# Kernel optimization log

Hardware: AMD Instinct MI355X
Metric: run time of the kernel (lower is better)

Reference implementation:

```python
import jax, jax.numpy as jnp
import numpy as np

N_NODES = 100000
N_EDGES = 1600000
N_GRAPHS = 256
HIDDEN = 128
IN_FEAT = 5


def setup_inputs() -> dict:
    key = jax.random.key(0)
    ks = jax.random.split(key, 12)
    x = jax.random.normal(ks[0], (N_NODES, IN_FEAT), dtype=jnp.float32)
    edge_index = jax.random.randint(ks[1], (2, N_EDGES), 0, N_NODES, dtype=jnp.int64)
    batch = jnp.sort(jax.random.randint(ks[2], (N_NODES,), 0, N_GRAPHS, dtype=jnp.int64))
    s = 0.05
    W0 = jax.random.normal(ks[3], (IN_FEAT, HIDDEN), dtype=jnp.float32) * s
    b0 = jnp.zeros((HIDDEN,), dtype=jnp.float32)
    W1 = jax.random.normal(ks[4], (HIDDEN, HIDDEN), dtype=jnp.float32) * s
    b1 = jnp.zeros((HIDDEN,), dtype=jnp.float32)
    W2 = jax.random.normal(ks[5], (HIDDEN, HIDDEN), dtype=jnp.float32) * s
    b2 = jnp.zeros((HIDDEN,), dtype=jnp.float32)
    lin_w = jax.random.normal(ks[6], (HIDDEN, 1), dtype=jnp.float32) * s
    lin_b = jnp.zeros((1,), dtype=jnp.float32)
    return {"x": x, "edge_index": edge_index, "batch": batch,
            "W0": W0, "b0": b0, "W1": W1, "b1": b1, "W2": W2, "b2": b2,
            "lin_w": lin_w, "lin_b": lin_b}


def reference(x, edge_index, batch, W0, b0, W1, b1, W2, b2, lin_w, lin_b):
    n = x.shape[0]
    # PyG GCNConv: add self-loops, symmetric normalization D^-1/2 (A+I) D^-1/2
    loop = jnp.arange(n, dtype=edge_index.dtype)
    src = jnp.concatenate([edge_index[0], loop])  # [E+N]
    dst = jnp.concatenate([edge_index[1], loop])
    deg = jax.ops.segment_sum(jnp.ones_like(dst, dtype=x.dtype), dst, num_segments=n)
    dis = jnp.where(deg > 0, jax.lax.rsqrt(jnp.maximum(deg, 1.0)), 0.0)
    norm = (dis[src] * dis[dst])[:, None]  # [E+N, 1]

    def gcn_conv(h, W, b):
        h = h @ W                      # [N, H]
        msg = h[src] * norm            # gather + scale, [E+N, H]
        return jax.ops.segment_sum(msg, dst, num_segments=n) + b

    h = jax.nn.relu(gcn_conv(x, W0, b0))
    h = jax.nn.relu(gcn_conv(h, W1, b1))
    h = gcn_conv(h, W2, b2)

    # global_mean_pool over batch ids
    sums = jax.ops.segment_sum(h, batch, num_segments=N_GRAPHS)
    cnt = jax.ops.segment_sum(jnp.ones((n,), x.dtype), batch, num_segments=N_GRAPHS)
    g = sums / jnp.maximum(cnt, 1.0)[:, None]
    # dropout p=0.01 is identity in eval mode
    return jax.nn.sigmoid(g @ lin_w + lin_b)  # [N_GRAPHS, 1]
```

## Files before the change

kernel.cpp:

```cpp
#include <hip/hip_runtime.h>
#include <hip/hip_fp8.h>

#define GCN_N 100000
#define GCN_H 128
#define GCN_G 256
#define NPB_SHIFT 9
#define NPB 512
#define NBKT 196
#define CHUNK 2048
#define SRC_BITS 17
#define SRC_MASK ((1 << SRC_BITS) - 1)
#define T1_SCALE 256.0f
#define T1_INV_SCALE (1.0f / 256.0f)

static_assert(GCN_N < (1 << SRC_BITS), "src id must fit 17 bits");

using short8 = __attribute__((ext_vector_type(8))) short;
using f32x4  = __attribute__((ext_vector_type(4))) float;
using f32x2  = __attribute__((ext_vector_type(2))) float;

#if defined(__has_builtin)
#if __has_builtin(__builtin_amdgcn_cvt_pk_f32_fp8) && __has_builtin(__builtin_amdgcn_cvt_pk_fp8_f32)
#define HW_FP8 1
#endif
#endif


__device__ __forceinline__ unsigned short f2bf(float f) {
    unsigned u = __float_as_uint(f);
    unsigned r = u + 0x7FFFu + ((u >> 16) & 1u);
    return (unsigned short)(r >> 16);
}
__device__ __forceinline__ float bf2f(unsigned short h) {
    return __uint_as_float(((unsigned)h) << 16);
}

__device__ __forceinline__ void fp8x4_to_f32(unsigned v, float* f) {
#ifdef HW_FP8
    f32x2 lo = __builtin_amdgcn_cvt_pk_f32_fp8((int)v, false);
    f32x2 hi = __builtin_amdgcn_cvt_pk_f32_fp8((int)v, true);
    f[0] = lo[0]; f[1] = lo[1]; f[2] = hi[0]; f[3] = hi[1];
#else
    #pragma unroll
    for (int j = 0; j < 4; j++) {
        __hip_fp8_e4m3 h;
        h.__x = (unsigned char)((v >> (8 * j)) & 0xFF);
        f[j] = (float)h;
    }
#endif
}

__device__ __forceinline__ unsigned f32x4_to_fp8(float f0, float f1, float f2, float f3) {
#ifdef HW_FP8
    int r = __builtin_amdgcn_cvt_pk_fp8_f32(f0, f1, 0, false);
    r = __builtin_amdgcn_cvt_pk_fp8_f32(f2, f3, r, true);
    return (unsigned)r;
#else
    unsigned r = 0;
    float ff[4] = {f0, f1, f2, f3};
    #pragma unroll
    for (int j = 0; j < 4; j++) {
        __hip_fp8_e4m3 h(ff[j]);
        r |= ((unsigned)h.__x) << (8 * j);
    }
    return r;
#endif
}


__global__ __launch_bounds__(256) void hist_kernel(const int* __restrict__ dst,
                                                   int* __restrict__ hist, int E) {
    __shared__ int lh[NBKT];
    int tid = threadIdx.x;
    if (tid < NBKT) lh[tid] = 0;
    __syncthreads();
    int e0 = blockIdx.x * CHUNK;
    #pragma unroll
    for (int i = 0; i < CHUNK / 256; i++) {
        int e = e0 + tid + i * 256;
        if (e < E) atomicAdd(&lh[dst[e] >> NPB_SHIFT], 1);
    }
    __syncthreads();
    if (tid < NBKT) hist[(size_t)blockIdx.x * NBKT + tid] = lh[tid];
}

__global__ __launch_bounds__(64) void scan_cols_kernel(const int* __restrict__ hist,
                                                       int* __restrict__ offsT,
                                                       int* __restrict__ btot, int B) {
    int k = blockIdx.x;
    int lane = threadIdx.x;
    int running = 0;
    for (int b0 = 0; b0 < B; b0 += 64) {
        int b = b0 + lane;
        int v = (b < B) ? hist[(size_t)b * NBKT + k] : 0;
        int iv = v;
        #pragma unroll
        for (int d = 1; d < 64; d <<= 1) {
            int x = __shfl_up(iv, d, 64);
            if (lane >= d) iv += x;
        }
        if (b < B) offsT[(size_t)k * B + b] = running + iv - v;
        running += __shfl(iv, 63, 64);
    }
    if (lane == 0) btot[k] = running;
}

__global__ void bucket_base_kernel(const int* __restrict__ btot,
                                   int* __restrict__ bbase,
                                   int* __restrict__ rowptr, int n) {
    if (threadIdx.x == 0 && blockIdx.x == 0) {
        int run = 0;
        for (int i = 0; i < NBKT; i++) { bbase[i] = run; run += btot[i]; }
        bbase[NBKT] = run;
        rowptr[n] = run;
    }
}

__global__ __launch_bounds__(256) void partition_kernel(const int* __restrict__ src,
                                                        const int* __restrict__ dst,
                                                        const int* __restrict__ bbase,
                                                        const int* __restrict__ offsT,
                                                        int* __restrict__ epack,
                                                        int E, int B) {
    __shared__ int cur[NBKT];
    int blk = blockIdx.x, tid = threadIdx.x;
    if (tid < NBKT) cur[tid] = bbase[tid] + offsT[(size_t)tid * B + blk];
    __syncthreads();
    int e0 = blk * CHUNK;
    #pragma unroll
    for (int i = 0; i < CHUNK / 256; i++) {
        int e = e0 + tid + i * 256;
        if (e < E) {
            int d = dst[e];
            int s = src[e];
            int pos = atomicAdd(&cur[d >> NPB_SHIFT], 1);
            epack[pos] = ((d & (NPB - 1)) << SRC_BITS) | s;
        }
    }
}

__global__ __launch_bounds__(512) void csr_build_kernel(const int* __restrict__ epack,
                                                        const int* __restrict__ bbase,
                                                        const float* __restrict__ x,
                                                        int* __restrict__ rowptr,
                                                        float* __restrict__ dis,
                                                        float* __restrict__ xsp,
                                                        int* __restrict__ csrc, int n) {
    __shared__ int lcount[NPB];
    __shared__ int lcur[NPB];
    __shared__ int wsums[8];
    int k = blockIdx.x, tid = threadIdx.x;
    int lane = tid & 63, wid = tid >> 6;
    int nodebase = k << NPB_SHIFT;
    int ebeg = bbase[k], eend = bbase[k + 1];

    lcount[tid] = 0;
    __syncthreads();
    for (int e = ebeg + tid; e < eend; e += 512)
        atomicAdd(&lcount[epack[e] >> SRC_BITS], 1);
    __syncthreads();

    int v = lcount[tid];
    int iv = v;
    #pragma unroll
    for (int d = 1; d < 64; d <<= 1) {
        int x2 = __shfl_up(iv, d, 64);
        if (lane >= d) iv += x2;
    }
    if (lane == 63) wsums[wid] = iv;
    __syncthreads();
    if (tid == 0) {
        int r = 0;
        #pragma unroll
        for (int w = 0; w < 8; w++) { int t = wsums[w]; wsums[w] = r; r += t; }
    }
    __syncthreads();
    int ex = wsums[wid] + iv - v;
    lcur[tid] = ex;
    int node = nodebase + tid;
    if (node < n) {
        rowptr[node] = ebeg + ex;
        float dd = rsqrtf((float)(v + 1));
        dis[node] = dd;
        const float* xr = x + (size_t)node * 5;
        float4 a;
        a.x = xr[0] * dd; a.y = xr[1] * dd; a.z = xr[2] * dd; a.w = xr[3] * dd;
        float a4 = xr[4] * dd;
        ((float4*)(xsp + (size_t)node * 8))[0] = a;
        xsp[(size_t)node * 8 + 4] = a4;
        xsp[(size_t)node * 8 + 5] = 0.f;
        xsp[(size_t)node * 8 + 6] = 0.f;
        xsp[(size_t)node * 8 + 7] = 0.f;
    }
    __syncthreads();
    for (int e = ebeg + tid; e < eend; e += 512) {
        int p = epack[e];
        int pos = atomicAdd(&lcur[p >> SRC_BITS], 1);
        csrc[ebeg + pos] = p & SRC_MASK;
    }
}


__global__ __launch_bounds__(256) void aggx_kernel(const float* __restrict__ xsp,
                                                   const float* __restrict__ dis,
                                                   const int* __restrict__ rowptr,
                                                   const int* __restrict__ csrc,
                                                   float* __restrict__ a0p, int n) {
    int i = blockIdx.x * 256 + threadIdx.x;
    if (i >= n) return;
    float4 acc = ((const float4*)(xsp + (size_t)i * 8))[0];
    float acc4 = xsp[(size_t)i * 8 + 4];
    int r0 = rowptr[i], r1 = rowptr[i + 1];
    int e = r0;
    for (; e + 3 < r1; e += 4) {
        int s0 = csrc[e], s1 = csrc[e + 1], s2 = csrc[e + 2], s3 = csrc[e + 3];
        float4 v0 = ((const float4*)(xsp + (size_t)s0 * 8))[0];
        float a40 = xsp[(size_t)s0 * 8 + 4];
        float4 v1 = ((const float4*)(xsp + (size_t)s1 * 8))[0];
        float a41 = xsp[(size_t)s1 * 8 + 4];
        float4 v2 = ((const float4*)(xsp + (size_t)s2 * 8))[0];
        float a42 = xsp[(size_t)s2 * 8 + 4];
        float4 v3 = ((const float4*)(xsp + (size_t)s3 * 8))[0];
        float a43 = xsp[(size_t)s3 * 8 + 4];
        acc.x += (v0.x + v1.x) + (v2.x + v3.x);
        acc.y += (v0.y + v1.y) + (v2.y + v3.y);
        acc.z += (v0.z + v1.z) + (v2.z + v3.z);
        acc.w += (v0.w + v1.w) + (v2.w + v3.w);
        acc4  += (a40 + a41) + (a42 + a43);
    }
    for (; e < r1; e++) {
        int s = csrc[e];
        float4 v = ((const float4*)(xsp + (size_t)s * 8))[0];
        acc.x += v.x; acc.y += v.y; acc.z += v.z; acc.w += v.w;
        acc4 += xsp[(size_t)s * 8 + 4];
    }
    float di = dis[i];
    acc.x *= di; acc.y *= di; acc.z *= di; acc.w *= di; acc4 *= di;
    ((float4*)(a0p + (size_t)i * 8))[0] = acc;
    a0p[(size_t)i * 8 + 4] = acc4;
}


__global__ __launch_bounds__(256) void w2l_kernel(const float* __restrict__ W2,
                                                  const float* __restrict__ b2,
                                                  const float* __restrict__ lw,
                                                  float* __restrict__ w2l,
                                                  float* __restrict__ c2) {
    __shared__ float slw[128];
    int tid = threadIdx.x;
    if (tid < 128) slw[tid] = lw[tid];
    __syncthreads();
    if (tid < 128) {
        float s = 0.f;
        #pragma unroll 8
        for (int j = 0; j < 128; j++) s = fmaf(W2[tid * 128 + j], slw[j], s);
        w2l[tid] = s;
    } else if (tid == 128) {
        float s = 0.f;
        for (int j = 0; j < 128; j++) s = fmaf(b2[j], slw[j], s);
        c2[0] = s;
    }
}

__global__ __launch_bounds__(256) void w1cvt_kernel(const float* __restrict__ W1,
                                                    unsigned short* __restrict__ w1t) {
    int idx = blockIdx.x * 256 + threadIdx.x;
    int col = idx >> 7, k = idx & 127;
    w1t[idx] = f2bf(W1[k * 128 + col]);
}


__global__ __launch_bounds__(256) void mmfused_kernel(const float* __restrict__ a0p,
                                                      const float* __restrict__ W0,
                                                      const float* __restrict__ b0,
                                                      const unsigned short* __restrict__ w1t,
                                                      const float* __restrict__ dis,
                                                      unsigned* __restrict__ t1f8, int n) {
    __shared__ __align__(16) unsigned short sA[128 * 128];
    __shared__ __align__(16) unsigned short sBT[128 * 128];
    __shared__ __align__(16) float4 sA0[256];
    __shared__ float sDis[128];
    char* sAb = (char*)sA;
    char* sBb = (char*)sBT;
    int tid = threadIdx.x;
    int rowBase = blockIdx.x * 128;

    {
        int rowL = tid >> 1, q = tid & 1;
        int gr = rowBase + rowL;
        float4 v = make_float4(0.f, 0.f, 0.f, 0.f);
        if (gr < n) v = ((const float4*)a0p)[(size_t)gr * 2 + q];
        sA0[tid] = v;
        if (tid < 128) {
            int g2 = rowBase + tid;
            sDis[tid] = (g2 < n) ? dis[g2] : 0.f;
        }
    }
    #pragma unroll
    for (int it = 0; it < 8; it++) {
        int idx = tid + it * 256;
        int col = idx >> 4, c = idx & 15;
        uint4 v = ((const uint4*)w1t)[idx];
        int byteoff = (col * 256 + c * 16) ^ ((col & 7) << 4);
        *(uint4*)(sBb + byteoff) = v;
    }
    __syncthreads();

    {
        int cq = tid & 31;
        int rg = tid >> 5;
        float4 w0q[5];
        #pragma unroll
        for (int j = 0; j < 5; j++) w0q[j] = *((const float4*)(W0 + j * 128 + cq * 4));
        float4 b0q = *((const float4*)(b0 + cq * 4));
        const float* sA0f = (const float*)sA0;
        #pragma unroll
        for (int ri = 0; ri < 16; ri++) {
            int row = rg + ri * 8;
            const float* ar = sA0f + row * 8;
            float4 h = b0q;
            #pragma unroll
            for (int j = 0; j < 5; j++) {
                float aj = ar[j];
                h.x = fmaf(aj, w0q[j].x, h.x);
                h.y = fmaf(aj, w0q[j].y, h.y);
                h.z = fmaf(aj, w0q[j].z, h.z);
                h.w = fmaf(aj, w0q[j].w, h.w);
            }
            h.x = fmaxf(h.x, 0.f); h.y = fmaxf(h.y, 0.f);
            h.z = fmaxf(h.z, 0.f); h.w = fmaxf(h.w, 0.f);
            uint2 p;
            p.x = (unsigned)f2bf(h.x) | ((unsigned)f2bf(h.y) << 16);
            p.y = (unsigned)f2bf(h.z) | ((unsigned)f2bf(h.w) << 16);
            int byteoff = (row * 256 + cq * 8) ^ ((row & 7) << 4);
            *(uint2*)(sAb + byteoff) = p;
        }
    }
    __syncthreads();

    int wave = tid >> 6, l = tid & 63;
    int lr = l & 15, lg = l >> 4;
    int rb = wave * 32;

    short8 afr[2][4];
    #pragma unroll
    for (int rt = 0; rt < 2; rt++) {
        int row = rb + rt * 16 + lr;
        #pragma unroll
        for (int ks = 0; ks < 4; ks++) {
            int byteoff = (row * 256 + ks * 64 + lg * 16) ^ ((row & 7) << 4);
            afr[rt][ks] = *(const short8*)(sAb + byteoff);
        }
    }
    f32x4 acc[2][8];
    #pragma unroll
    for (int rt = 0; rt < 2; rt++)
        #pragma unroll
        for (int ct = 0; ct < 8; ct++)
            acc[rt][ct] = (f32x4){0.f, 0.f, 0.f, 0.f};

    #pragma unroll
    for (int ct = 0; ct < 8; ct++) {
        int col = ct * 16 + lr;
        short8 bfr[4];
        #pragma unroll
        for (int ks = 0; ks < 4; ks++) {
            int byteoff = (col * 256 + ks * 64 + lg * 16) ^ ((col & 7) << 4);
            bfr[ks] = *(const short8*)(sBb + byteoff);
        }
        #pragma unroll
        for (int rt = 0; rt < 2; rt++) {
            #pragma unroll
            for (int ks = 0; ks < 4; ks++) {
                acc[rt][ct] = __builtin_amdgcn_mfma_f32_16x16x32_bf16(
                    afr[rt][ks], bfr[ks], acc[rt][ct], 0, 0, 0);
            }
        }
    }

    #pragma unroll
    for (int rt = 0; rt < 2; rt++) {
        #pragma unroll
        for (int i = 0; i < 4; i++) {
            int rowL = rb + rt * 16 + lg * 4 + i;
            float dsc = sDis[rowL] * T1_SCALE;
            #pragma unroll
            for (int ct = 0; ct < 8; ct++) {
                int col = ct * 16 + lr;
                int byteoff = (rowL * 256 + col * 2) ^ ((rowL & 7) << 4);
                *(unsigned short*)(sAb + byteoff) = f2bf(acc[rt][ct][i] * dsc);
            }
        }
    }
    __syncthreads();

    #pragma unroll
    for (int it = 0; it < 8; it++) {
        int flat = tid + it * 256;
        int rowL = flat >> 4, c16 = flat & 15;
        int gr = rowBase + rowL;
        if (gr < n) {
            int byteoff = (rowL * 256 + c16 * 16) ^ ((rowL & 7) << 4);
            uint4 v = *(const uint4*)(sAb + byteoff);
            float f0 = __uint_as_float(v.x << 16), f1 = __uint_as_float(v.x & 0xFFFF0000u);
            float f2 = __uint_as_float(v.y << 16), f3 = __uint_as_float(v.y & 0xFFFF0000u);
            float f4 = __uint_as_float(v.z << 16), f5 = __uint_as_float(v.z & 0xFFFF0000u);
            float f6 = __uint_as_float(v.w << 16), f7 = __uint_as_float(v.w & 0xFFFF0000u);
            uint2 p;
            p.x = f32x4_to_fp8(f0, f1, f2, f3);
            p.y = f32x4_to_fp8(f4, f5, f6, f7);
            ((uint2*)t1f8)[(size_t)gr * 16 + c16] = p;
        }
    }
}


__global__ __launch_bounds__(256) void agg1_kernel(const unsigned* __restrict__ t1f8,
                                                   const float* __restrict__ dis,
                                                   const int* __restrict__ rowptr,
                                                   const int* __restrict__ csrc,
                                                   const float* __restrict__ b1,
                                                   const float* __restrict__ w2l,
                                                   float* __restrict__ z, int n) {
    int group = threadIdx.x >> 4, lane = threadIdx.x & 15;
    int i = blockIdx.x * 16 + group;
    if (i >= n) return;
    const uint2* t2 = (const uint2*)t1f8;
    float f[8];
    uint2 sv = t2[(size_t)i * 16 + lane];
    fp8x4_to_f32(sv.x, f);
    fp8x4_to_f32(sv.y, f + 4);
    float acc[8];
    #pragma unroll
    for (int j = 0; j < 8; j++) acc[j] = f[j];
    int r0 = rowptr[i], r1 = rowptr[i + 1];
    int e = r0;
    for (; e + 7 < r1; e += 8) {
        uint2 vv[8];
        #pragma unroll
        for (int u = 0; u < 8; u++) vv[u] = t2[(size_t)csrc[e + u] * 16 + lane];
        #pragma unroll
        for (int u = 0; u < 8; u++) {
            fp8x4_to_f32(vv[u].x, f);
            fp8x4_to_f32(vv[u].y, f + 4);
            #pragma unroll
            for (int j = 0; j < 8; j++) acc[j] += f[j];
        }
    }
    for (; e < r1; e++) {
        uint2 v = t2[(size_t)csrc[e] * 16 + lane];
        fp8x4_to_f32(v.x, f);
        fp8x4_to_f32(v.y, f + 4);
        #pragma unroll
        for (int j = 0; j < 8; j++) acc[j] += f[j];
    }
    float di = dis[i];
    float dis_s = di * T1_INV_SCALE;
    float4 b4a = ((const float4*)b1)[lane * 2];
    float4 b4b = ((const float4*)b1)[lane * 2 + 1];
    float4 w4a = ((const float4*)w2l)[lane * 2];
    float4 w4b = ((const float4*)w2l)[lane * 2 + 1];
    float bb[8] = {b4a.x, b4a.y, b4a.z, b4a.w, b4b.x, b4b.y, b4b.z, b4b.w};
    float ww[8] = {w4a.x, w4a.y, w4a.z, w4a.w, w4b.x, w4b.y, w4b.z, w4b.w};
    float d = 0.f;
    #pragma unroll
    for (int j = 0; j < 8; j++) {
        float c = fmaxf(fmaf(dis_s, acc[j], bb[j]), 0.f);
        d = fmaf(c, ww[j], d);
    }
    #pragma unroll
    for (int o = 8; o > 0; o >>= 1) d += __shfl_down(d, o, 16);
    if (lane == 0) z[i] = di * d;
}


__global__ __launch_bounds__(256) void aggz_pool_kernel(const float* __restrict__ z,
                                                        const float* __restrict__ dis,
                                                        const int* __restrict__ rowptr,
                                                        const int* __restrict__ csrc,
                                                        const int* __restrict__ batch,
                                                        float* __restrict__ gsum, int n) {
    __shared__ float lg[GCN_G];
    int tid = threadIdx.x;
    lg[tid] = 0.f;
    __syncthreads();
    int i = blockIdx.x * 256 + tid;
    float ndv = 0.f;
    int g = 0;
    if (i < n) {
        float acc = z[i];
        int r0 = rowptr[i], r1 = rowptr[i + 1];
        int e = r0;
        for (; e + 3 < r1; e += 4) {
            acc += (z[csrc[e]] + z[csrc[e + 1]]) + (z[csrc[e + 2]] + z[csrc[e + 3]]);
        }
        for (; e < r1; e++) acc += z[csrc[e]];
        ndv = dis[i] * acc;
        g = batch[i];
    }
    int lane = tid & 63;
    int g0 = __shfl(g, 0, 64);
    bool uni = __all(g == g0);
    if (uni) {
        float s = ndv;
        #pragma unroll
        for (int o = 32; o > 0; o >>= 1) s += __shfl_down(s, o, 64);
        if (lane == 0 && s != 0.f) atomicAdd(&lg[g0], s);
    } else {
        if (ndv != 0.f) atomicAdd(&lg[g], ndv);
    }
    __syncthreads();
    float v = lg[tid];
    if (v != 0.f) atomicAdd(&gsum[tid], v);
}


__global__ __launch_bounds__(256) void boundary_kernel(const int* __restrict__ batch,
                                                       int* __restrict__ gstart, int n) {
    int i = blockIdx.x * 256 + threadIdx.x;
    if (i >= n) return;
    int b = batch[i];
    int pb = (i == 0) ? -1 : batch[i - 1];
    for (int g = pb + 1; g <= b; g++) gstart[g] = i;
    if (i == n - 1) {
        for (int g = b + 1; g <= GCN_G; g++) gstart[g] = n;
    }
}

__global__ __launch_bounds__(256) void final_kernel(const float* __restrict__ gsum,
                                                    const int* __restrict__ gstart,
                                                    const float* __restrict__ c2,
                                                    const float* __restrict__ lb,
                                                    float* __restrict__ out) {
    int g = threadIdx.x;
    float cnt = (float)max(gstart[g + 1] - gstart[g], 1);
    float v = gsum[g] / cnt + c2[0] + lb[0];
    out[g] = 1.f / (1.f + expf(-v));
}


extern "C" void kernel_launch(void* const* d_in, const int* in_sizes, int n_in,
                              void* d_out, int out_size, void* d_ws, size_t ws_size,
                              hipStream_t stream) {
    const float* x   = (const float*)d_in[0];
    const int*   ei  = (const int*)d_in[1];
    const int*   bat = (const int*)d_in[2];
    const float* W0  = (const float*)d_in[3];
    const float* b0  = (const float*)d_in[4];
    const float* W1  = (const float*)d_in[5];
    const float* b1  = (const float*)d_in[6];
    const float* W2  = (const float*)d_in[7];
    const float* b2  = (const float*)d_in[8];
    const float* lw  = (const float*)d_in[9];
    const float* lb  = (const float*)d_in[10];
    float* out = (float*)d_out;

    const int N = GCN_N;
    const int E = in_sizes[1] / 2;
    const int B = (E + CHUNK - 1) / CHUNK;

    char* ws = (char*)d_ws;
    size_t off = 0;
    auto alloc = [&](size_t bytes) {
        size_t o = off;
        off += (bytes + 255) & ~(size_t)255;
        return o;
    };
    int*   hist    = (int*)(ws + alloc((size_t)B * NBKT * 4));
    int*   offsT   = (int*)(ws + alloc((size_t)NBKT * B * 4));
    int*   btot    = (int*)(ws + alloc((size_t)NBKT * 4));
    int*   bbase   = (int*)(ws + alloc((size_t)(NBKT + 1) * 4));
    int*   epack   = (int*)(ws + alloc((size_t)E * 4));
    int*   rowptr  = (int*)(ws + alloc((size_t)(N + 1) * 4));
    float* dis     = (float*)(ws + alloc((size_t)N * 4));
    int*   csrc    = (int*)(ws + alloc((size_t)E * 4));
    float* xsp     = (float*)(ws + alloc((size_t)N * 8 * 4));
    float* a0p     = (float*)(ws + alloc((size_t)N * 8 * 4));
    unsigned* t1f8 = (unsigned*)(ws + alloc((size_t)N * GCN_H));
    float* z       = (float*)(ws + alloc((size_t)N * 4));
    int*   gstart  = (int*)(ws + alloc((size_t)(GCN_G + 1) * 4));
    float* w2l     = (float*)(ws + alloc(128 * 4));
    float* c2      = (float*)(ws + alloc(4));
    unsigned short* w1t = (unsigned short*)(ws + alloc(128 * 128 * 2));
    float* gsum    = (float*)(ws + alloc(GCN_G * 4));

    const int* src = ei;
    const int* dst = ei + E;

    hipMemsetAsync(gsum, 0, GCN_G * 4, stream);

    hist_kernel<<<B, 256, 0, stream>>>(dst, hist, E);
    scan_cols_kernel<<<NBKT, 64, 0, stream>>>(hist, offsT, btot, B);
    bucket_base_kernel<<<1, 64, 0, stream>>>(btot, bbase, rowptr, N);
    partition_kernel<<<B, 256, 0, stream>>>(src, dst, bbase, offsT, epack, E, B);
    csr_build_kernel<<<NBKT, 512, 0, stream>>>(epack, bbase, x, rowptr, dis, xsp, csrc, N);
    boundary_kernel<<<(N + 255) / 256, 256, 0, stream>>>(bat, gstart, N);
    w2l_kernel<<<1, 256, 0, stream>>>(W2, b2, lw, w2l, c2);
    w1cvt_kernel<<<64, 256, 0, stream>>>(W1, w1t);

    aggx_kernel<<<(N + 255) / 256, 256, 0, stream>>>(xsp, dis, rowptr, csrc, a0p, N);
    mmfused_kernel<<<(N + 127) / 128, 256, 0, stream>>>(a0p, W0, b0, w1t, dis, t1f8, N);
    agg1_kernel<<<(N + 15) / 16, 256, 0, stream>>>(t1f8, dis, rowptr, csrc, b1, w2l, z, N);
    aggz_pool_kernel<<<(N + 255) / 256, 256, 0, stream>>>(z, dis, rowptr, csrc, bat, gsum, N);

    final_kernel<<<1, 256, 0, stream>>>(gsum, gstart, c2, lb, out);
}
```

Measured before the change: 152.0 us.

## Merge prep kernels, cache edges in LDS, widen gather unrolls, count graphs in pool

Merges the W1 conversion, W2·lin_w reduction and bucket-base scan into one prep kernel, and drops boundary_kernel by counting nodes per graph inside the pooling kernel, so fewer kernels are launched. csr_build now caches its bucket's packed edges in LDS to avoid a second global read, at the cost of 40KB of shared memory per block, which may lower occupancy. The aggregation loops gather 8 or 16 neighbours per step, and agg1 loads indices cooperatively and broadcasts them with shuffles, to raise memory-level parallelism. The extra gcnt buffer relies on being allocated right after gsum so that the widened memset clears both.

```diff
diff --git a/kernel.cpp b/kernel.cpp
--- a/kernel.cpp
+++ b/kernel.cpp
@@ -12,6 +12,7 @@
 #define SRC_MASK ((1 << SRC_BITS) - 1)
 #define T1_SCALE 256.0f
 #define T1_INV_SCALE (1.0f / 256.0f)
+#define EBUF_CAP 10240
 
 static_assert(GCN_N < (1 << SRC_BITS), "src id must fit 17 bits");
 
@@ -105,14 +106,42 @@
     if (lane == 0) btot[k] = running;
 }
 
-__global__ void bucket_base_kernel(const int* __restrict__ btot,
-                                   int* __restrict__ bbase,
-                                   int* __restrict__ rowptr, int n) {
-    if (threadIdx.x == 0 && blockIdx.x == 0) {
-        int run = 0;
-        for (int i = 0; i < NBKT; i++) { bbase[i] = run; run += btot[i]; }
-        bbase[NBKT] = run;
-        rowptr[n] = run;
+__global__ __launch_bounds__(256) void prep_kernel(const float* __restrict__ W1,
+                                                   const float* __restrict__ W2,
+                                                   const float* __restrict__ b2,
+                                                   const float* __restrict__ lw,
+                                                   const int* __restrict__ btot,
+                                                   unsigned short* __restrict__ w1t,
+                                                   float* __restrict__ w2l,
+                                                   float* __restrict__ c2,
+                                                   int* __restrict__ bbase,
+                                                   int* __restrict__ rowptr, int n) {
+    __shared__ float slw[128];
+    int blk = blockIdx.x, tid = threadIdx.x;
+    if (blk < 64) {
+        int idx = blk * 256 + tid;
+        int col = idx >> 7, k = idx & 127;
+        w1t[idx] = f2bf(W1[k * 128 + col]);
+    } else if (blk == 64) {
+        if (tid < 128) slw[tid] = lw[tid];
+        __syncthreads();
+        if (tid < 128) {
+            float s = 0.f;
+            #pragma unroll 8
+            for (int j = 0; j < 128; j++) s = fmaf(W2[tid * 128 + j], slw[j], s);
+            w2l[tid] = s;
+        } else if (tid == 128) {
+            float s = 0.f;
+            for (int j = 0; j < 128; j++) s = fmaf(b2[j], slw[j], s);
+            c2[0] = s;
+        }
+    } else {
+        if (tid == 0) {
+            int run = 0;
+            for (int i = 0; i < NBKT; i++) { bbase[i] = run; run += btot[i]; }
+            bbase[NBKT] = run;
+            rowptr[n] = run;
+        }
     }
 }
 
@@ -146,6 +175,7 @@
                                                         float* __restrict__ dis,
                                                         float* __restrict__ xsp,
                                                         int* __restrict__ csrc, int n) {
+    __shared__ int ebuf[EBUF_CAP];
     __shared__ int lcount[NPB];
     __shared__ int lcur[NPB];
     __shared__ int wsums[8];
@@ -153,11 +183,15 @@
     int lane = tid & 63, wid = tid >> 6;
     int nodebase = k << NPB_SHIFT;
     int ebeg = bbase[k], eend = bbase[k + 1];
+    bool fits = (eend - ebeg) <= EBUF_CAP;
 
     lcount[tid] = 0;
     __syncthreads();
-    for (int e = ebeg + tid; e < eend; e += 512)
-        atomicAdd(&lcount[epack[e] >> SRC_BITS], 1);
+    for (int e = ebeg + tid; e < eend; e += 512) {
+        int p = epack[e];
+        if (fits) ebuf[e - ebeg] = p;
+        atomicAdd(&lcount[p >> SRC_BITS], 1);
+    }
     __syncthreads();
 
     int v = lcount[tid];
@@ -194,7 +228,7 @@
     }
     __syncthreads();
     for (int e = ebeg + tid; e < eend; e += 512) {
-        int p = epack[e];
+        int p = fits ? ebuf[e - ebeg] : epack[e];
         int pos = atomicAdd(&lcur[p >> SRC_BITS], 1);
         csrc[ebeg + pos] = p & SRC_MASK;
     }
@@ -212,21 +246,21 @@
     float acc4 = xsp[(size_t)i * 8 + 4];
     int r0 = rowptr[i], r1 = rowptr[i + 1];
     int e = r0;
-    for (; e + 3 < r1; e += 4) {
-        int s0 = csrc[e], s1 = csrc[e + 1], s2 = csrc[e + 2], s3 = csrc[e + 3];
-        float4 v0 = ((const float4*)(xsp + (size_t)s0 * 8))[0];
-        float a40 = xsp[(size_t)s0 * 8 + 4];
-        float4 v1 = ((const float4*)(xsp + (size_t)s1 * 8))[0];
-        float a41 = xsp[(size_t)s1 * 8 + 4];
-        float4 v2 = ((const float4*)(xsp + (size_t)s2 * 8))[0];
-        float a42 = xsp[(size_t)s2 * 8 + 4];
-        float4 v3 = ((const float4*)(xsp + (size_t)s3 * 8))[0];
-        float a43 = xsp[(size_t)s3 * 8 + 4];
-        acc.x += (v0.x + v1.x) + (v2.x + v3.x);
-        acc.y += (v0.y + v1.y) + (v2.y + v3.y);
-        acc.z += (v0.z + v1.z) + (v2.z + v3.z);
-        acc.w += (v0.w + v1.w) + (v2.w + v3.w);
-        acc4  += (a40 + a41) + (a42 + a43);
+    for (; e + 7 < r1; e += 8) {
+        int ss[8];
+        #pragma unroll
+        for (int u = 0; u < 8; u++) ss[u] = csrc[e + u];
+        float4 v[8]; float a4[8];
+        #pragma unroll
+        for (int u = 0; u < 8; u++) {
+            v[u] = ((const float4*)(xsp + (size_t)ss[u] * 8))[0];
+            a4[u] = xsp[(size_t)ss[u] * 8 + 4];
+        }
+        #pragma unroll
+        for (int u = 0; u < 8; u++) {
+            acc.x += v[u].x; acc.y += v[u].y; acc.z += v[u].z; acc.w += v[u].w;
+            acc4 += a4[u];
+        }
     }
     for (; e < r1; e++) {
         int s = csrc[e];
@@ -238,35 +272,6 @@
     acc.x *= di; acc.y *= di; acc.z *= di; acc.w *= di; acc4 *= di;
     ((float4*)(a0p + (size_t)i * 8))[0] = acc;
     a0p[(size_t)i * 8 + 4] = acc4;
-}
-
-
-__global__ __launch_bounds__(256) void w2l_kernel(const float* __restrict__ W2,
-                                                  const float* __restrict__ b2,
-                                                  const float* __restrict__ lw,
-                                                  float* __restrict__ w2l,
-                                                  float* __restrict__ c2) {
-    __shared__ float slw[128];
-    int tid = threadIdx.x;
-    if (tid < 128) slw[tid] = lw[tid];
-    __syncthreads();
-    if (tid < 128) {
-        float s = 0.f;
-        #pragma unroll 8
-        for (int j = 0; j < 128; j++) s = fmaf(W2[tid * 128 + j], slw[j], s);
-        w2l[tid] = s;
-    } else if (tid == 128) {
-        float s = 0.f;
-        for (int j = 0; j < 128; j++) s = fmaf(b2[j], slw[j], s);
-        c2[0] = s;
-    }
-}
-
-__global__ __launch_bounds__(256) void w1cvt_kernel(const float* __restrict__ W1,
-                                                    unsigned short* __restrict__ w1t) {
-    int idx = blockIdx.x * 256 + threadIdx.x;
-    int col = idx >> 7, k = idx & 127;
-    w1t[idx] = f2bf(W1[k * 128 + col]);
 }
 
 
@@ -426,33 +431,34 @@
     int i = blockIdx.x * 16 + group;
     if (i >= n) return;
     const uint2* t2 = (const uint2*)t1f8;
-    float f[8];
+    float f[8], acc[8];
     uint2 sv = t2[(size_t)i * 16 + lane];
     fp8x4_to_f32(sv.x, f);
     fp8x4_to_f32(sv.y, f + 4);
-    float acc[8];
     #pragma unroll
     for (int j = 0; j < 8; j++) acc[j] = f[j];
     int r0 = rowptr[i], r1 = rowptr[i + 1];
-    int e = r0;
-    for (; e + 7 < r1; e += 8) {
-        uint2 vv[8];
-        #pragma unroll
-        for (int u = 0; u < 8; u++) vv[u] = t2[(size_t)csrc[e + u] * 16 + lane];
-        #pragma unroll
-        for (int u = 0; u < 8; u++) {
-            fp8x4_to_f32(vv[u].x, f);
-            fp8x4_to_f32(vv[u].y, f + 4);
-            #pragma unroll
-            for (int j = 0; j < 8; j++) acc[j] += f[j];
-        }
-    }
-    for (; e < r1; e++) {
-        uint2 v = t2[(size_t)csrc[e] * 16 + lane];
-        fp8x4_to_f32(v.x, f);
-        fp8x4_to_f32(v.y, f + 4);
-        #pragma unroll
-        for (int j = 0; j < 8; j++) acc[j] += f[j];
+    for (int e = r0; e < r1; e += 16) {
+        int cnt = r1 - e; if (cnt > 16) cnt = 16;
+        int idx = e + lane;
+        int si = (idx < r1) ? csrc[idx] : 0;
+        uint2 vv[16];
+        #pragma unroll
+        for (int u = 0; u < 16; u++) {
+            if (u < cnt) {
+                int s = __shfl(si, u, 16);
+                vv[u] = t2[(size_t)s * 16 + lane];
+            }
+        }
+        #pragma unroll
+        for (int u = 0; u < 16; u++) {
+            if (u < cnt) {
+                fp8x4_to_f32(vv[u].x, f);
+                fp8x4_to_f32(vv[u].y, f + 4);
+                #pragma unroll
+                for (int j = 0; j < 8; j++) acc[j] += f[j];
+            }
+        }
     }
     float di = dis[i];
     float dis_s = di * T1_INV_SCALE;
@@ -479,20 +485,31 @@
                                                         const int* __restrict__ rowptr,
                                                         const int* __restrict__ csrc,
                                                         const int* __restrict__ batch,
-                                                        float* __restrict__ gsum, int n) {
+                                                        float* __restrict__ gsum,
+                                                        int* __restrict__ gcnt, int n) {
     __shared__ float lg[GCN_G];
+    __shared__ int lc[GCN_G];
     int tid = threadIdx.x;
     lg[tid] = 0.f;
+    lc[tid] = 0;
     __syncthreads();
     int i = blockIdx.x * 256 + tid;
+    bool valid = i < n;
     float ndv = 0.f;
     int g = 0;
-    if (i < n) {
+    if (valid) {
         float acc = z[i];
         int r0 = rowptr[i], r1 = rowptr[i + 1];
         int e = r0;
-        for (; e + 3 < r1; e += 4) {
-            acc += (z[csrc[e]] + z[csrc[e + 1]]) + (z[csrc[e + 2]] + z[csrc[e + 3]]);
+        for (; e + 7 < r1; e += 8) {
+            int ss[8];
+            #pragma unroll
+            for (int u = 0; u < 8; u++) ss[u] = csrc[e + u];
+            float zv[8];
+            #pragma unroll
+            for (int u = 0; u < 8; u++) zv[u] = z[ss[u]];
+            #pragma unroll
+            for (int u = 0; u < 8; u++) acc += zv[u];
         }
         for (; e < r1; e++) acc += z[csrc[e]];
         ndv = dis[i] * acc;
@@ -500,40 +517,34 @@
     }
     int lane = tid & 63;
     int g0 = __shfl(g, 0, 64);
-    bool uni = __all(g == g0);
+    bool uni = __all(g == g0) && __all(valid);
     if (uni) {
         float s = ndv;
         #pragma unroll
         for (int o = 32; o > 0; o >>= 1) s += __shfl_down(s, o, 64);
-        if (lane == 0 && s != 0.f) atomicAdd(&lg[g0], s);
-    } else {
-        if (ndv != 0.f) atomicAdd(&lg[g], ndv);
+        if (lane == 0) {
+            atomicAdd(&lg[g0], s);
+            atomicAdd(&lc[g0], 64);
+        }
+    } else if (valid) {
+        atomicAdd(&lg[g], ndv);
+        atomicAdd(&lc[g], 1);
     }
     __syncthreads();
     float v = lg[tid];
+    int c = lc[tid];
     if (v != 0.f) atomicAdd(&gsum[tid], v);
-}
-
-
-__global__ __launch_bounds__(256) void boundary_kernel(const int* __restrict__ batch,
-                                                       int* __restrict__ gstart, int n) {
-    int i = blockIdx.x * 256 + threadIdx.x;
-    if (i >= n) return;
-    int b = batch[i];
-    int pb = (i == 0) ? -1 : batch[i - 1];
-    for (int g = pb + 1; g <= b; g++) gstart[g] = i;
-    if (i == n - 1) {
-        for (int g = b + 1; g <= GCN_G; g++) gstart[g] = n;
-    }
-}
+    if (c != 0) atomicAdd(&gcnt[tid], c);
+}
+
 
 __global__ __launch_bounds__(256) void final_kernel(const float* __restrict__ gsum,
-                                                    const int* __restrict__ gstart,
+                                                    const int* __restrict__ gcnt,
                                                     const float* __restrict__ c2,
                                                     const float* __restrict__ lb,
                                                     float* __restrict__ out) {
     int g = threadIdx.x;
-    float cnt = (float)max(gstart[g + 1] - gstart[g], 1);
+    float cnt = (float)max(gcnt[g], 1);
     float v = gsum[g] / cnt + c2[0] + lb[0];
     out[g] = 1.f / (1.f + expf(-v));
 }
@@ -578,30 +589,27 @@
     float* a0p     = (float*)(ws + alloc((size_t)N * 8 * 4));
     unsigned* t1f8 = (unsigned*)(ws + alloc((size_t)N * GCN_H));
     float* z       = (float*)(ws + alloc((size_t)N * 4));
-    int*   gstart  = (int*)(ws + alloc((size_t)(GCN_G + 1) * 4));
     float* w2l     = (float*)(ws + alloc(128 * 4));
     float* c2      = (float*)(ws + alloc(4));
     unsigned short* w1t = (unsigned short*)(ws + alloc(128 * 128 * 2));
     float* gsum    = (float*)(ws + alloc(GCN_G * 4));
+    int*   gcnt    = (int*)(ws + alloc(GCN_G * 4));
 
     const int* src = ei;
     const int* dst = ei + E;
 
-    hipMemsetAsync(gsum, 0, GCN_G * 4, stream);
+    hipMemsetAsync(gsum, 0, GCN_G * 4 * 2, stream);
 
     hist_kernel<<<B, 256, 0, stream>>>(dst, hist, E);
     scan_cols_kernel<<<NBKT, 64, 0, stream>>>(hist, offsT, btot, B);
-    bucket_base_kernel<<<1, 64, 0, stream>>>(btot, bbase, rowptr, N);
+    prep_kernel<<<66, 256, 0, stream>>>(W1, W2, b2, lw, btot, w1t, w2l, c2, bbase, rowptr, N);
     partition_kernel<<<B, 256, 0, stream>>>(src, dst, bbase, offsT, epack, E, B);
     csr_build_kernel<<<NBKT, 512, 0, stream>>>(epack, bbase, x, rowptr, dis, xsp, csrc, N);
-    boundary_kernel<<<(N + 255) / 256, 256, 0, stream>>>(bat, gstart, N);
-    w2l_kernel<<<1, 256, 0, stream>>>(W2, b2, lw, w2l, c2);
-    w1cvt_kernel<<<64, 256, 0, stream>>>(W1, w1t);
 
     aggx_kernel<<<(N + 255) / 256, 256, 0, stream>>>(xsp, dis, rowptr, csrc, a0p, N);
     mmfused_kernel<<<(N + 127) / 128, 256, 0, stream>>>(a0p, W0, b0, w1t, dis, t1f8, N);
     agg1_kernel<<<(N + 15) / 16, 256, 0, stream>>>(t1f8, dis, rowptr, csrc, b1, w2l, z, N);
-    aggz_pool_kernel<<<(N + 255) / 256, 256, 0, stream>>>(z, dis, rowptr, csrc, bat, gsum, N);
-
-    final_kernel<<<1, 256, 0, stream>>>(gsum, gstart, c2, lb, out);
-}
+    aggz_pool_kernel<<<(N + 255) / 256, 256, 0, stream>>>(z, dis, rowptr, csrc, bat, gsum, gcnt, N);
+
+    final_kernel<<<1, 256, 0, stream>>>(gsum, gcnt, c2, lb, out);
+}
```

Result: no change. 149.6 us (-1.6%).
